# Performance work log

Hardware: AMD Instinct MI355X
Metric: run time of the kernel (lower is better)

## Reference

```python
import jax, jax.numpy as jnp
import numpy as np

N = 50000      # nodes
E = 800000     # edges (avg degree 16)
C = 32         # channels per degree (deg0 and deg1)
HRAD = 32      # radial MLP hidden
L = 4          # attention layers (plus 1 output layer)
HEADS = 4
EPS = 1e-6
NRAD = 7 * C   # rk00, rk10, rv00, rv10, rv11, rv01, rv11b


def setup_inputs() -> dict:
    key = jax.random.key(0)
    ks = jax.random.split(key, 16)
    L1 = L + 1
    s = 0.1
    return {
        "pos": jax.random.normal(ks[0], (N, 3), jnp.float32),
        "f0": jax.random.normal(ks[1], (N, C), jnp.float32),
        "f1": jax.random.normal(ks[2], (N, C, 3), jnp.float32),
        "src": jax.random.randint(ks[3], (E,), 0, N, jnp.int32),
        "dst": jax.random.randint(ks[4], (E,), 0, N, jnp.int32),
        "W1": jax.random.normal(ks[5], (L1, 1, HRAD), jnp.float32) * s,
        "b1": jnp.zeros((L1, HRAD), jnp.float32),
        "W2": jax.random.normal(ks[6], (L1, HRAD, NRAD), jnp.float32) * s,
        "b2": jnp.zeros((L1, NRAD), jnp.float32),
        "Wq": jax.random.normal(ks[7], (L1, C, C), jnp.float32) * s,
        "Wo0": jax.random.normal(ks[8], (L1, C, C), jnp.float32) * s,
        "Wo1": jax.random.normal(ks[9], (L1, C, C), jnp.float32) * s,
        "Ws0": jax.random.normal(ks[10], (L1, C, C), jnp.float32) * s,
        "Ws1": jax.random.normal(ks[11], (L1, C, C), jnp.float32) * s,
        "bg": jnp.zeros((L, C), jnp.float32),
    }


def _attn_layer(f0, f1, u, rlen, src, dst, n, heads,
                W1, b1, W2, b2, Wq, Wo0, Wo1, Ws0, Ws1):
    # radial network, channel-wise modulation per interaction path
    h = jax.nn.relu(rlen[:, None] @ W1 + b1)            # [E, HRAD]
    R = h @ W2 + b2                                     # [E, 7C]
    rk00, rk10, rv00, rv10, rv11, rv01, rv11b = jnp.split(R, 7, axis=-1)
    f0s = f0[src]                                       # [E, C]
    f1s = f1[src]                                       # [E, C, 3]
    dot1 = jnp.einsum('ecd,ed->ec', f1s, u)             # deg1 -> invariant [E, C]
    # equivariant keys (deg0) and values (deg0 + deg1)
    k0 = rk00 * f0s + rk10 * dot1                       # [E, C]
    v0 = rv00 * f0s + rv10 * dot1                       # [E, C]
    v1 = rv11[..., None] * f1s + (rv01 * f0s + rv11b * dot1)[..., None] * u[:, None, :]  # [E, C, 3]
    # multi-head attention logits on invariants
    ch = C // heads
    q = (f0 @ Wq)[dst].reshape(-1, heads, ch)           # [E, H, ch]
    kh = k0.reshape(-1, heads, ch)
    logits = (q * kh).sum(-1) / np.sqrt(ch)             # [E, H]
    # segment softmax over incoming edges of each dst node
    m = jax.ops.segment_max(logits, dst, num_segments=n)
    e = jnp.exp(logits - m[dst])
    z = jax.ops.segment_sum(e, dst, num_segments=n)
    alpha = e / (z[dst] + EPS)                          # [E, H]
    ac = jnp.repeat(alpha, ch, axis=1)                  # [E, C]
    o0 = jax.ops.segment_sum(ac * v0, dst, num_segments=n)                  # [N, C]
    o1 = jax.ops.segment_sum(ac[..., None] * v1, dst, num_segments=n)       # [N, C, 3]
    # self-interaction + skip
    out0 = o0 @ Wo0 + f0 @ Ws0
    out1 = jnp.einsum('ncd,ce->ned', o1, Wo1) + jnp.einsum('ncd,ce->ned', f1, Ws1)
    return out0, out1


def _forward(pos, f0, f1, src, dst, W1, b1, W2, b2, Wq, Wo0, Wo1, Ws0, Ws1, bg):
    n = f0.shape[0]
    # edge-wise basis (l=0,1 spherical harmonics ~ unit direction) and radial distance
    rel = pos[dst] - pos[src]                           # [E, 3]
    rlen = jnp.linalg.norm(rel, axis=-1)                # [E]
    u = rel / (rlen + EPS)[:, None]                     # [E, 3]
    for i in range(L):
        f0, f1 = _attn_layer(f0, f1, u, rlen, src, dst, n, HEADS,
                             W1[i], b1[i], W2[i], b2[i], Wq[i],
                             Wo0[i], Wo1[i], Ws0[i], Ws1[i])
        # GProjRelu: relu on invariants, norm-gated relu on deg-1
        f0 = jax.nn.relu(f0)
        n1 = jnp.linalg.norm(f1, axis=-1)               # [N, C]
        f1 = f1 * (jax.nn.relu(n1 + bg[i]) / (n1 + EPS))[..., None]
    # final output layer: single head, no nonlinearity
    f0, f1 = _attn_layer(f0, f1, u, rlen, src, dst, n, 1,
                         W1[L], b1[L], W2[L], b2[L], Wq[L],
                         Wo0[L], Wo1[L], Ws0[L], Ws1[L])
    return f0, f1


def reference(pos, f0, f1, src, dst, W1, b1, W2, b2, Wq, Wo0, Wo1, Ws0, Ws1, bg):
    return _forward(pos, f0, f1, src, dst, W1, b1, W2, b2, Wq, Wo0, Wo1, Ws0, Ws1, bg)
```

## Files before the change

kernel.cpp:

```cpp
#include <hip/hip_runtime.h>
#include <math.h>

#define CCH 32
#define NCH 224
#define NIV 33
#define HRAD 32
#define ET 16
#define DG1 48


__global__ void hist_kernel(const int* __restrict__ dst, int* __restrict__ counts, int E) {
  int e = blockIdx.x * 256 + threadIdx.x;
  if (e < E) atomicAdd(&counts[dst[e]], 1);
}

__global__ void scan1_kernel(const int* __restrict__ counts, int* __restrict__ offs,
                             int* __restrict__ bsums, int n) {
  __shared__ int sd[1024];
  int t = threadIdx.x;
  int i = blockIdx.x * 1024 + t;
  int v = (i < n) ? counts[i] : 0;
  sd[t] = v;
  __syncthreads();
  for (int o = 1; o < 1024; o <<= 1) {
    int add = (t >= o) ? sd[t - o] : 0;
    __syncthreads();
    sd[t] += add;
    __syncthreads();
  }
  if (i < n) offs[i] = sd[t] - v;
  if (t == 1023) bsums[blockIdx.x] = sd[1023];
}

__global__ void scan2_kernel(int* bsums, int nb) {
  if (threadIdx.x == 0 && blockIdx.x == 0) {
    int acc = 0;
    for (int i = 0; i < nb; i++) { int v = bsums[i]; bsums[i] = acc; acc += v; }
  }
}

__global__ void scan3_kernel(int* __restrict__ offs, const int* __restrict__ bsums,
                             int* __restrict__ cursor, int n, int E) {
  int i = blockIdx.x * 256 + threadIdx.x;
  if (i < n) {
    int v = offs[i] + bsums[i >> 10];
    offs[i] = v;
    cursor[i] = v;
  } else if (i == n) {
    offs[n] = E;
  }
}

__global__ void scatter_kernel(const float* __restrict__ pos, const int* __restrict__ src,
                               const int* __restrict__ dst, int* __restrict__ cursor,
                               int* __restrict__ esrcS, float4* __restrict__ egeoS, int E) {
  int e = blockIdx.x * 256 + threadIdx.x;
  if (e >= E) return;
  int s = src[e], d = dst[e];
  float rx = pos[d * 3 + 0] - pos[s * 3 + 0];
  float ry = pos[d * 3 + 1] - pos[s * 3 + 1];
  float rz = pos[d * 3 + 2] - pos[s * 3 + 2];
  float rl = sqrtf(rx * rx + ry * ry + rz * rz);
  float inv = 1.0f / (rl + 1e-6f);
  int p = atomicAdd(&cursor[d], 1);
  esrcS[p] = s;
  egeoS[p] = make_float4(rx * inv, ry * inv, rz * inv, rl);
}


__global__ void deghistA_kernel(const int* __restrict__ counts, int* __restrict__ bbase,
                                int n, int cpb) {
  __shared__ int lh[256];
  int t = threadIdx.x;
  lh[t] = 0;
  __syncthreads();
  int s = blockIdx.x * cpb, e = s + cpb; if (e > n) e = n;
  for (int i = s + t; i < e; i += 256) {
    int d = counts[i]; d = d > 255 ? 255 : d;
    atomicAdd(&lh[d], 1);
  }
  __syncthreads();
  bbase[blockIdx.x * 256 + t] = lh[t];
}

__global__ void degscanB_kernel(int* __restrict__ bbase) {
  __shared__ int sM[DG1 * 256];
  __shared__ int gb[256];
  int t = threadIdx.x;
  for (int i = t; i < DG1 * 256; i += 256) sM[i] = bbase[i];
  __syncthreads();
  int tot = 0;
  for (int b = 0; b < DG1; b++) tot += sM[b * 256 + t];
  gb[t] = tot;
  __syncthreads();
  if (t == 0) {
    int acc = 0;
    for (int d = 255; d >= 0; --d) { int v = gb[d]; gb[d] = acc; acc += v; }
  }
  __syncthreads();
  int run = gb[t];
  for (int b = 0; b < DG1; b++) { int v = sM[b * 256 + t]; sM[b * 256 + t] = run; run += v; }
  __syncthreads();
  for (int i = t; i < DG1 * 256; i += 256) bbase[i] = sM[i];
}

__global__ void degscatC_kernel(const int* __restrict__ counts, const int* __restrict__ bbase,
                                int* __restrict__ perm, int n, int cpb) {
  __shared__ int lc[256];
  int t = threadIdx.x;
  lc[t] = bbase[blockIdx.x * 256 + t];
  __syncthreads();
  int s = blockIdx.x * cpb, e = s + cpb; if (e > n) e = n;
  for (int i = s + t; i < e; i += 256) {
    int d = counts[i]; d = d > 255 ? 255 : d;
    int p = atomicAdd(&lc[d], 1);
    perm[p] = i;
  }
}


__global__ void pwl_build_kernel(const float* __restrict__ W1, const float* __restrict__ b1,
                                 const float* __restrict__ W2, const float* __restrict__ b2,
                                 float2* __restrict__ coef, float* __restrict__ tks) {
  int l = blockIdx.x / NIV;
  int iv = blockIdx.x - l * NIV;
  int tid = threadIdx.x;
  const float* w1 = W1 + l * HRAD;
  const float* bb1 = b1 + l * HRAD;
  const float* w2 = W2 + l * HRAD * NCH;
  const float* bb2 = b2 + l * NCH;
  __shared__ float a_s[HRAD], b_s[HRAD], t_s[HRAD], t_sorted[HRAD];
  if (tid < HRAD) {
    float a = w1[tid], b = bb1[tid];
    a_s[tid] = a; b_s[tid] = b;
    t_s[tid] = (a != 0.0f) ? (-b / a) : 1e30f;
  }
  __syncthreads();
  if (tid < HRAD) {
    float tj = t_s[tid];
    int rank = 0;
    for (int k = 0; k < HRAD; k++) {
      float tk = t_s[k];
      rank += (tk < tj) || (tk == tj && k < tid);
    }
    t_sorted[rank] = tj;
    if (iv == 0) tks[l * HRAD + tid] = tj;
  }
  __syncthreads();
  if (tid < NCH) {
    int k = tid;
    double lo = (iv == 0) ? (double)t_sorted[0] - 1.0 : (double)t_sorted[iv - 1];
    double hi = (iv == NIV - 1) ? (double)t_sorted[HRAD - 1] + 1.0 : (double)t_sorted[iv];
    double rm = 0.5 * (lo + hi);
    if (iv == 0) rm = (double)t_sorted[0] - 1.0;
    if (iv == NIV - 1) rm = (double)t_sorted[HRAD - 1] + 1.0;
    float alpha = bb2[k];
    float beta = 0.0f;
    for (int j = 0; j < HRAD; j++) {
      if ((double)a_s[j] * rm + (double)b_s[j] > 0.0) {
        float w = w2[j * NCH + k];
        alpha = fmaf(w, b_s[j], alpha);
        beta = fmaf(w, a_s[j], beta);
      }
    }
    coef[l * (NIV * NCH) + iv * NCH + (k & 31) * 7 + (k >> 5)] = make_float2(alpha, beta);
  }
}


__global__ __launch_bounds__(512) void pack_kernel(
    const float* __restrict__ f0, const float* __restrict__ f1,
    const float* __restrict__ Wq0, float scale0,
    float4* __restrict__ fpk, float* __restrict__ qbuf, int n) {
  __shared__ float sWq[1024];
  __shared__ float sF0[ET * 32];
  int tid = threadIdx.x;
  for (int i = tid; i < 1024; i += 512) sWq[i] = Wq0[i];
  __syncthreads();
  int nl = tid >> 5, c = tid & 31;
  for (int base = blockIdx.x * ET; base < n; base += gridDim.x * ET) {
    int node = base + nl;
    float v0 = 0.f, x = 0.f, y = 0.f, z = 0.f;
    if (node < n) {
      v0 = f0[(size_t)node * 32 + c];
      size_t b = ((size_t)node * 32 + c) * 3;
      x = f1[b]; y = f1[b + 1]; z = f1[b + 2];
      fpk[(size_t)node * 32 + c] = make_float4(v0, x, y, z);
    }
    sF0[nl * 32 + c] = v0;
    __syncthreads();
    if (node < n) {
      float q = 0.f;
#pragma unroll
      for (int k = 0; k < 32; k++) q = fmaf(sF0[nl * 32 + k], sWq[k * 32 + c], q);
      qbuf[(size_t)node * 32 + c] = q * scale0;
    }
    __syncthreads();
  }
}


template<int CTRL>
__device__ __forceinline__ float dpp_xor_add(float t) {
  return t + __int_as_float(__builtin_amdgcn_update_dpp(
      0, __float_as_int(t), CTRL, 0xF, 0xF, true));
}

template<int CH>
__global__ __launch_bounds__(1024) void node_kernel(
    const float4* __restrict__ fpk, const float* __restrict__ qbuf,
    float4* __restrict__ Opk,
    const int* __restrict__ esrcS, const float4* __restrict__ egeoS,
    const int* __restrict__ offs, const int* __restrict__ perm,
    const float2* __restrict__ coefG, const float* __restrict__ tkG,
    int n) {
  __shared__ float2 sCoef[NIV * NCH];
  __shared__ float sTk[CCH];
  int tid = threadIdx.x;
  for (int i = tid; i < NIV * NCH; i += 1024) sCoef[i] = coefG[i];
  if (tid < CCH) sTk[tid] = tkG[tid];
  __syncthreads();

  int lane = tid & 63;
  int wid = tid >> 6;
  int c = lane & 31;
  int half = lane >> 5;
  float tk_c = sTk[c];

  int W = gridDim.x * 16;
  int gw = blockIdx.x * 16 + wid;

  int pos0 = gw;
  int pos1 = 2 * W - 1 - gw;
  int pos2 = 2 * W + gw;
  int kk = 2;

  int pcur = (pos0 < n) ? perm[pos0] : 0;
  int pnext = (pos1 < n) ? perm[pos1] : 0;
  int start = 0, end = 0;
  float qs = 0.f;
  int pA = 0;
  float4 pgA = make_float4(0, 0, 0, 0);
  if (pos0 < n) {
    start = offs[pcur];
    end = offs[pcur + 1];
    qs = qbuf[pcur * 32 + c];
    int j0 = start + half;
    if (j0 < end) { pA = esrcS[j0]; pgA = egeoS[j0]; }
  }

  for (; pos0 < n; ) {
    int pnn = (pos2 < n) ? perm[pos2] : 0;
    int nstart = 0, nend = 0;
    float nqs = 0.f;
    if (pos1 < n) {
      nstart = offs[pnext];
      nend = offs[pnext + 1];
      nqs = qbuf[pnext * 32 + c];
    }

    float z = 0.0f;
    float o0 = 0.0f, o10 = 0.0f, o11 = 0.0f, o12 = 0.0f;

    int j = start + half;
    int sB = 0;
    float4 gA = pgA, gB = make_float4(0, 0, 0, 0);
    float4 FA = make_float4(0, 0, 0, 0);
    if (j < end) {
      FA = fpk[pA * 32 + c];
    }
    if (j + 2 < end) { sB = esrcS[j + 2]; gB = egeoS[j + 2]; }

    unsigned long long msk = __ballot(gA.w > tk_c);
    int iv = half ? (int)__popcll(msk >> 32) : (int)__popcll(msk & 0xFFFFFFFFull);
    const float2* cf = sCoef + (iv * 32 + c) * 7;
    float2 cq0 = cf[0], cq1 = cf[1], cq2 = cf[2], cq3 = cf[3];
    float2 cq4 = cf[4], cq5 = cf[5], cq6 = cf[6];

    while (j < end) {
      float4 g = gA;
      float4 F = FA;
      float2 q0 = cq0, q1 = cq1, q2 = cq2, q3 = cq3;
      float2 q4 = cq4, q5 = cq5, q6 = cq6;
      int j2 = j + 2;
      if (j2 < end) {
        FA = fpk[sB * 32 + c];
        gA = gB;
        if (j2 + 2 < end) { sB = esrcS[j2 + 2]; gB = egeoS[j2 + 2]; }
      }
      msk = __ballot(gA.w > tk_c);
      iv = half ? (int)__popcll(msk >> 32) : (int)__popcll(msk & 0xFFFFFFFFull);
      cf = sCoef + (iv * 32 + c) * 7;
      cq0 = cf[0]; cq1 = cf[1]; cq2 = cf[2]; cq3 = cf[3];
      cq4 = cf[4]; cq5 = cf[5]; cq6 = cf[6];

      float r = g.w;
      float rk00 = fmaf(q0.y, r, q0.x), rk10 = fmaf(q1.y, r, q1.x);
      float rv00 = fmaf(q2.y, r, q2.x), rv10 = fmaf(q3.y, r, q3.x);
      float rv11 = fmaf(q4.y, r, q4.x), rv01 = fmaf(q5.y, r, q5.x);
      float rv11b = fmaf(q6.y, r, q6.x);
      float dot1 = fmaf(F.y, g.x, fmaf(F.z, g.y, F.w * g.z));
      float k0 = fmaf(rk00, F.x, rk10 * dot1);
      float t = qs * k0;
      t = dpp_xor_add<0xB1>(t);
      t = dpp_xor_add<0x4E>(t);
      t = dpp_xor_add<0x141>(t);
      if constexpr (CH == 32) {
        t = dpp_xor_add<0x140>(t);
        t = t + __int_as_float(__builtin_amdgcn_ds_swizzle(
                __float_as_int(t), 0x401F));
      }
      float p = __builtin_amdgcn_exp2f(t);
      z += p;
      float v0 = fmaf(rv00, F.x, rv10 * dot1);
      float sg = fmaf(rv01, F.x, rv11b * dot1);
      o0  = fmaf(p, v0, o0);
      o10 = fmaf(p, fmaf(rv11, F.y, sg * g.x), o10);
      o11 = fmaf(p, fmaf(rv11, F.z, sg * g.y), o11);
      o12 = fmaf(p, fmaf(rv11, F.w, sg * g.z), o12);
      j = j2;
    }

    pA = 0;
    pgA = make_float4(0, 0, 0, 0);
    if (pos1 < n) {
      int nj = nstart + half;
      if (nj < nend) { pA = esrcS[nj]; pgA = egeoS[nj]; }
    }

    float zo  = __shfl_xor(z, 32, 64);
    float p0  = __shfl_xor(o0, 32, 64);
    float p10 = __shfl_xor(o10, 32, 64);
    float p11 = __shfl_xor(o11, 32, 64);
    float p12 = __shfl_xor(o12, 32, 64);
    float zf = z + zo;
    float inv = 1.0f / (zf + 1e-6f);
    if (!half) {
      Opk[pcur * 32 + c] = make_float4(
          (o0 + p0) * inv,
          (o10 + p10) * inv,
          (o11 + p11) * inv,
          (o12 + p12) * inv);
    }

    pcur = pnext;
    pnext = pnn;
    start = nstart;
    end = nend;
    qs = nqs;
    pos0 = pos1;
    pos1 = pos2;
    ++kk;
    pos2 = kk * W + ((kk & 1) ? (W - 1 - gw) : gw);
  }
}


__global__ __launch_bounds__(512) void epi_kernel(
    const float4* __restrict__ Opk, float4* __restrict__ fpk,
    const float* __restrict__ Wo0G, const float* __restrict__ Ws0G,
    const float* __restrict__ Wo1G, const float* __restrict__ Ws1G,
    const float* __restrict__ bgG,
    const float* __restrict__ WqN, float* __restrict__ qbuf, float scaleN,
    float* __restrict__ out0, float* __restrict__ out1,
    int mode, int n) {
  __shared__ float4 sW[32 * 32];
  __shared__ float  sWq[32 * 32];
  __shared__ float4 sO[ET * 32];
  __shared__ float4 sF[ET * 32];
  __shared__ float  sF0[ET * 32];
  int tid = threadIdx.x;
  for (int i = tid; i < 1024; i += 512) {
    sW[i] = make_float4(Wo0G[i], Ws0G[i], Wo1G[i], Ws1G[i]);
    if (mode == 0) sWq[i] = WqN[i];
  }
  __syncthreads();
  int nl = tid >> 5;
  int c  = tid & 31;
  for (int base = blockIdx.x * ET; base < n; base += gridDim.x * ET) {
    int node = base + nl;
    bool valid = node < n;
    if (valid) {
      sO[tid] = Opk[(size_t)node * 32 + c];
      sF[tid] = fpk[(size_t)node * 32 + c];
    }
    __syncthreads();
    float a0 = 0.f, ax = 0.f, ay = 0.f, az = 0.f;
#pragma unroll
    for (int k = 0; k < 32; k++) {
      float4 O = sO[nl * 32 + k];
      float4 F = sF[nl * 32 + k];
      float4 w = sW[k * 32 + c];
      a0 = fmaf(O.x, w.x, fmaf(F.x, w.y, a0));
      ax = fmaf(O.y, w.z, fmaf(F.y, w.w, ax));
      ay = fmaf(O.z, w.z, fmaf(F.z, w.w, ay));
      az = fmaf(O.w, w.z, fmaf(F.w, w.w, az));
    }
    if (mode == 0) {
      float f0n = fmaxf(a0, 0.f);
      float n1 = sqrtf(fmaf(ax, ax, fmaf(ay, ay, az * az)));
      float gate = fmaxf(n1 + bgG[c], 0.f) / (n1 + 1e-6f);
      if (valid) fpk[(size_t)node * 32 + c] = make_float4(f0n, ax * gate, ay * gate, az * gate);
      sF0[nl * 32 + c] = f0n;
      __syncthreads();
      if (valid) {
        float q = 0.f;
#pragma unroll
        for (int k = 0; k < 32; k++) q = fmaf(sF0[nl * 32 + k], sWq[k * 32 + c], q);
        qbuf[(size_t)node * 32 + c] = q * scaleN;
      }
      __syncthreads();
    } else {
      if (valid) {
        out0[(size_t)node * 32 + c] = a0;
        size_t b = ((size_t)node * 32 + c) * 3;
        out1[b] = ax; out1[b + 1] = ay; out1[b + 2] = az;
      }
      __syncthreads();
    }
  }
}


extern "C" void kernel_launch(void* const* d_in, const int* in_sizes, int n_in,
                              void* d_out, int out_size, void* d_ws, size_t ws_size,
                              hipStream_t stream) {
  const float* pos = (const float*)d_in[0];
  const float* f0  = (const float*)d_in[1];
  const float* f1  = (const float*)d_in[2];
  const int* src   = (const int*)d_in[3];
  const int* dst   = (const int*)d_in[4];
  const float* W1  = (const float*)d_in[5];
  const float* b1  = (const float*)d_in[6];
  const float* W2  = (const float*)d_in[7];
  const float* b2  = (const float*)d_in[8];
  const float* Wq  = (const float*)d_in[9];
  const float* Wo0 = (const float*)d_in[10];
  const float* Wo1 = (const float*)d_in[11];
  const float* Ws0 = (const float*)d_in[12];
  const float* Ws1 = (const float*)d_in[13];
  const float* bg  = (const float*)d_in[14];

  int N = in_sizes[0] / 3;
  int E = in_sizes[3];

  char* p = (char*)d_ws;
  auto alloc = [&](size_t bytes) {
    char* r = p;
    p += (bytes + 255) & ~(size_t)255;
    return r;
  };
  int* counts   = (int*)alloc((size_t)N * 4);
  int* offs     = (int*)alloc((size_t)(N + 1) * 4);
  int* cursor   = (int*)alloc((size_t)N * 4);
  int* bsums    = (int*)alloc(1024 * 4);
  int* esrcS    = (int*)alloc((size_t)E * 4);
  float4* egeoS = (float4*)alloc((size_t)E * 16);
  float2* coef  = (float2*)alloc((size_t)5 * NIV * NCH * 8);
  float* tks    = (float*)alloc((size_t)5 * HRAD * 4);
  float4* fpk   = (float4*)alloc((size_t)N * CCH * 16);
  float4* Opk   = (float4*)alloc((size_t)N * CCH * 16);
  float* qbuf   = (float*)alloc((size_t)N * CCH * 4);
  int* bbase    = (int*)alloc((size_t)DG1 * 256 * 4);
  int* perm     = (int*)alloc((size_t)N * 4);

  int cpb = (N + DG1 - 1) / DG1;

  pwl_build_kernel<<<5 * NIV, 256, 0, stream>>>(W1, b1, W2, b2, coef, tks);
  hipMemsetAsync(counts, 0, (size_t)N * 4, stream);
  hist_kernel<<<(E + 255) / 256, 256, 0, stream>>>(dst, counts, E);
  deghistA_kernel<<<DG1, 256, 0, stream>>>(counts, bbase, N, cpb);
  int nb = (N + 1023) / 1024;
  scan1_kernel<<<nb, 1024, 0, stream>>>(counts, offs, bsums, N);
  scan2_kernel<<<1, 64, 0, stream>>>(bsums, nb);
  scan3_kernel<<<(N + 1 + 255) / 256, 256, 0, stream>>>(offs, bsums, cursor, N, E);
  degscanB_kernel<<<1, 256, 0, stream>>>(bbase);
  degscatC_kernel<<<DG1, 256, 0, stream>>>(counts, bbase, perm, N, cpb);
  scatter_kernel<<<(E + 255) / 256, 256, 0, stream>>>(pos, src, dst, cursor, esrcS, egeoS, E);

  const float LOG2E = 1.4426950408889634f;
  float sc8 = LOG2E / sqrtf(8.0f);
  float sc32 = LOG2E / sqrtf(32.0f);
  int nblk = (N + ET - 1) / ET;
  pack_kernel<<<nblk, 512, 0, stream>>>(f0, f1, Wq, sc8, fpk, qbuf, N);

  float* out0 = (float*)d_out;
  float* out1 = out0 + (size_t)N * CCH;
  for (int l = 0; l < 5; l++) {
    bool last = (l == 4);
    if (last) {
      node_kernel<32><<<512, 1024, 0, stream>>>(
          fpk, qbuf, Opk, esrcS, egeoS, offs, perm,
          coef + (size_t)l * NIV * NCH, tks + l * HRAD, N);
    } else {
      node_kernel<8><<<512, 1024, 0, stream>>>(
          fpk, qbuf, Opk, esrcS, egeoS, offs, perm,
          coef + (size_t)l * NIV * NCH, tks + l * HRAD, N);
    }
    epi_kernel<<<nblk, 512, 0, stream>>>(
        Opk, fpk,
        Wo0 + l * CCH * CCH, Ws0 + l * CCH * CCH,
        Wo1 + l * CCH * CCH, Ws1 + l * CCH * CCH,
        bg + (last ? 0 : l) * CCH,
        Wq + (l + 1 <= 4 ? (l + 1) : 4) * CCH * CCH, qbuf,
        (l + 1 == 4) ? sc32 : sc8,
        out0, out1, last ? 1 : 0, N);
  }
}
```

Before: 776.0 us.

## Precompute per-edge radial interval indices for all layers in scatter

The scatter kernel now counts, for every edge and each of the five layers, how many radial-MLP breakpoints its length exceeds. It packs these five 6-bit interval indices next to the source index in an int2 array. The node kernel then reads the interval index directly instead of doing a per-edge ballot and popcount against per-channel thresholds. It also evaluates the piecewise-linear radial coefficients one edge ahead in the software pipeline, which trims the critical path of the inner loop. The cost is a larger per-edge record (8 bytes instead of 4) and extra comparison work in the one-time scatter pass.

```diff
diff --git a/kernel.cpp b/kernel.cpp
--- a/kernel.cpp
+++ b/kernel.cpp
@@ -51,10 +51,16 @@
   }
 }
 
+
 __global__ void scatter_kernel(const float* __restrict__ pos, const int* __restrict__ src,
                                const int* __restrict__ dst, int* __restrict__ cursor,
-                               int* __restrict__ esrcS, float4* __restrict__ egeoS, int E) {
-  int e = blockIdx.x * 256 + threadIdx.x;
+                               const float* __restrict__ tksAll,
+                               int2* __restrict__ epkS, float4* __restrict__ egeoS, int E) {
+  __shared__ float sT[5 * HRAD];
+  int t = threadIdx.x;
+  if (t < 5 * HRAD) sT[t] = tksAll[t];
+  __syncthreads();
+  int e = blockIdx.x * 256 + t;
   if (e >= E) return;
   int s = src[e], d = dst[e];
   float rx = pos[d * 3 + 0] - pos[s * 3 + 0];
@@ -62,8 +68,16 @@
   float rz = pos[d * 3 + 2] - pos[s * 3 + 2];
   float rl = sqrtf(rx * rx + ry * ry + rz * rz);
   float inv = 1.0f / (rl + 1e-6f);
+  int ivpk = 0;
+#pragma unroll
+  for (int l = 0; l < 5; l++) {
+    int cnt = 0;
+#pragma unroll
+    for (int k = 0; k < HRAD; k++) cnt += (rl > sT[l * HRAD + k]) ? 1 : 0;
+    ivpk |= cnt << (6 * l);
+  }
   int p = atomicAdd(&cursor[d], 1);
-  esrcS[p] = s;
+  epkS[p] = make_int2(s, ivpk);
   egeoS[p] = make_float4(rx * inv, ry * inv, rz * inv, rl);
 }
 
@@ -210,22 +224,19 @@
 __global__ __launch_bounds__(1024) void node_kernel(
     const float4* __restrict__ fpk, const float* __restrict__ qbuf,
     float4* __restrict__ Opk,
-    const int* __restrict__ esrcS, const float4* __restrict__ egeoS,
+    const int2* __restrict__ epkS, const float4* __restrict__ egeoS,
     const int* __restrict__ offs, const int* __restrict__ perm,
-    const float2* __restrict__ coefG, const float* __restrict__ tkG,
+    const float2* __restrict__ coefG, int ivshift,
     int n) {
   __shared__ float2 sCoef[NIV * NCH];
-  __shared__ float sTk[CCH];
   int tid = threadIdx.x;
   for (int i = tid; i < NIV * NCH; i += 1024) sCoef[i] = coefG[i];
-  if (tid < CCH) sTk[tid] = tkG[tid];
   __syncthreads();
 
   int lane = tid & 63;
   int wid = tid >> 6;
   int c = lane & 31;
   int half = lane >> 5;
-  float tk_c = sTk[c];
 
   int W = gridDim.x * 16;
   int gw = blockIdx.x * 16 + wid;
@@ -239,14 +250,14 @@
   int pnext = (pos1 < n) ? perm[pos1] : 0;
   int start = 0, end = 0;
   float qs = 0.f;
-  int pA = 0;
-  float4 pgA = make_float4(0, 0, 0, 0);
+  int2 pe = make_int2(0, 0);
+  float4 pg = make_float4(0, 0, 0, 0);
   if (pos0 < n) {
     start = offs[pcur];
     end = offs[pcur + 1];
     qs = qbuf[pcur * 32 + c];
     int j0 = start + half;
-    if (j0 < end) { pA = esrcS[j0]; pgA = egeoS[j0]; }
+    if (j0 < end) { pe = epkS[j0]; pg = egeoS[j0]; }
   }
 
   for (; pos0 < n; ) {
@@ -263,45 +274,50 @@
     float o0 = 0.0f, o10 = 0.0f, o11 = 0.0f, o12 = 0.0f;
 
     int j = start + half;
-    int sB = 0;
-    float4 gA = pgA, gB = make_float4(0, 0, 0, 0);
-    float4 FA = make_float4(0, 0, 0, 0);
+
+    float4 g = pg;
+    float4 F = make_float4(0, 0, 0, 0);
+    float R0 = 0, R1 = 0, R2 = 0, R3 = 0, R4 = 0, R5 = 0, R6 = 0;
+    int2 e1 = make_int2(0, 0);
+    float4 g1 = make_float4(0, 0, 0, 0);
     if (j < end) {
-      FA = fpk[pA * 32 + c];
-    }
-    if (j + 2 < end) { sB = esrcS[j + 2]; gB = egeoS[j + 2]; }
-
-    unsigned long long msk = __ballot(gA.w > tk_c);
-    int iv = half ? (int)__popcll(msk >> 32) : (int)__popcll(msk & 0xFFFFFFFFull);
-    const float2* cf = sCoef + (iv * 32 + c) * 7;
-    float2 cq0 = cf[0], cq1 = cf[1], cq2 = cf[2], cq3 = cf[3];
-    float2 cq4 = cf[4], cq5 = cf[5], cq6 = cf[6];
+      F = fpk[pe.x * 32 + c];
+      int iv = (pe.y >> ivshift) & 63;
+      const float2* cf = sCoef + (iv * 32 + c) * 7;
+      float r = g.w;
+      R0 = fmaf(cf[0].y, r, cf[0].x);
+      R1 = fmaf(cf[1].y, r, cf[1].x);
+      R2 = fmaf(cf[2].y, r, cf[2].x);
+      R3 = fmaf(cf[3].y, r, cf[3].x);
+      R4 = fmaf(cf[4].y, r, cf[4].x);
+      R5 = fmaf(cf[5].y, r, cf[5].x);
+      R6 = fmaf(cf[6].y, r, cf[6].x);
+    }
+    if (j + 2 < end) { e1 = epkS[j + 2]; g1 = egeoS[j + 2]; }
 
     while (j < end) {
-      float4 g = gA;
-      float4 F = FA;
-      float2 q0 = cq0, q1 = cq1, q2 = cq2, q3 = cq3;
-      float2 q4 = cq4, q5 = cq5, q6 = cq6;
+      float4 gc = g;
+      float4 Fc = F;
+      float r0 = R0, r1 = R1, r2 = R2, r3 = R3, r4 = R4, r5 = R5, r6 = R6;
       int j2 = j + 2;
       if (j2 < end) {
-        FA = fpk[sB * 32 + c];
-        gA = gB;
-        if (j2 + 2 < end) { sB = esrcS[j2 + 2]; gB = egeoS[j2 + 2]; }
+        F = fpk[e1.x * 32 + c];
+        int iv = (e1.y >> ivshift) & 63;
+        const float2* cf = sCoef + (iv * 32 + c) * 7;
+        float r = g1.w;
+        R0 = fmaf(cf[0].y, r, cf[0].x);
+        R1 = fmaf(cf[1].y, r, cf[1].x);
+        R2 = fmaf(cf[2].y, r, cf[2].x);
+        R3 = fmaf(cf[3].y, r, cf[3].x);
+        R4 = fmaf(cf[4].y, r, cf[4].x);
+        R5 = fmaf(cf[5].y, r, cf[5].x);
+        R6 = fmaf(cf[6].y, r, cf[6].x);
+        g = g1;
+        if (j2 + 2 < end) { e1 = epkS[j2 + 2]; g1 = egeoS[j2 + 2]; }
       }
-      msk = __ballot(gA.w > tk_c);
-      iv = half ? (int)__popcll(msk >> 32) : (int)__popcll(msk & 0xFFFFFFFFull);
-      cf = sCoef + (iv * 32 + c) * 7;
-      cq0 = cf[0]; cq1 = cf[1]; cq2 = cf[2]; cq3 = cf[3];
-      cq4 = cf[4]; cq5 = cf[5]; cq6 = cf[6];
-
-      float r = g.w;
-      float rk00 = fmaf(q0.y, r, q0.x), rk10 = fmaf(q1.y, r, q1.x);
-      float rv00 = fmaf(q2.y, r, q2.x), rv10 = fmaf(q3.y, r, q3.x);
-      float rv11 = fmaf(q4.y, r, q4.x), rv01 = fmaf(q5.y, r, q5.x);
-      float rv11b = fmaf(q6.y, r, q6.x);
-      float dot1 = fmaf(F.y, g.x, fmaf(F.z, g.y, F.w * g.z));
-      float k0 = fmaf(rk00, F.x, rk10 * dot1);
-      float t = qs * k0;
+
+      float dot1 = fmaf(Fc.y, gc.x, fmaf(Fc.z, gc.y, Fc.w * gc.z));
+      float t = qs * fmaf(r0, Fc.x, r1 * dot1);
       t = dpp_xor_add<0xB1>(t);
       t = dpp_xor_add<0x4E>(t);
       t = dpp_xor_add<0x141>(t);
@@ -312,20 +328,20 @@
       }
       float p = __builtin_amdgcn_exp2f(t);
       z += p;
-      float v0 = fmaf(rv00, F.x, rv10 * dot1);
-      float sg = fmaf(rv01, F.x, rv11b * dot1);
+      float v0 = fmaf(r2, Fc.x, r3 * dot1);
+      float sg = fmaf(r5, Fc.x, r6 * dot1);
       o0  = fmaf(p, v0, o0);
-      o10 = fmaf(p, fmaf(rv11, F.y, sg * g.x), o10);
-      o11 = fmaf(p, fmaf(rv11, F.z, sg * g.y), o11);
-      o12 = fmaf(p, fmaf(rv11, F.w, sg * g.z), o12);
+      o10 = fmaf(p, fmaf(r4, Fc.y, sg * gc.x), o10);
+      o11 = fmaf(p, fmaf(r4, Fc.z, sg * gc.y), o11);
+      o12 = fmaf(p, fmaf(r4, Fc.w, sg * gc.z), o12);
       j = j2;
     }
 
-    pA = 0;
-    pgA = make_float4(0, 0, 0, 0);
+    pe = make_int2(0, 0);
+    pg = make_float4(0, 0, 0, 0);
     if (pos1 < n) {
       int nj = nstart + half;
-      if (nj < nend) { pA = esrcS[nj]; pgA = egeoS[nj]; }
+      if (nj < nend) { pe = epkS[nj]; pg = egeoS[nj]; }
     }
 
     float zo  = __shfl_xor(z, 32, 64);
@@ -454,7 +470,7 @@
   int* offs     = (int*)alloc((size_t)(N + 1) * 4);
   int* cursor   = (int*)alloc((size_t)N * 4);
   int* bsums    = (int*)alloc(1024 * 4);
-  int* esrcS    = (int*)alloc((size_t)E * 4);
+  int2* epkS    = (int2*)alloc((size_t)E * 8);
   float4* egeoS = (float4*)alloc((size_t)E * 16);
   float2* coef  = (float2*)alloc((size_t)5 * NIV * NCH * 8);
   float* tks    = (float*)alloc((size_t)5 * HRAD * 4);
@@ -476,7 +492,8 @@
   scan3_kernel<<<(N + 1 + 255) / 256, 256, 0, stream>>>(offs, bsums, cursor, N, E);
   degscanB_kernel<<<1, 256, 0, stream>>>(bbase);
   degscatC_kernel<<<DG1, 256, 0, stream>>>(counts, bbase, perm, N, cpb);
-  scatter_kernel<<<(E + 255) / 256, 256, 0, stream>>>(pos, src, dst, cursor, esrcS, egeoS, E);
+  scatter_kernel<<<(E + 255) / 256, 256, 0, stream>>>(pos, src, dst, cursor, tks,
+                                                      epkS, egeoS, E);
 
   const float LOG2E = 1.4426950408889634f;
   float sc8 = LOG2E / sqrtf(8.0f);
@@ -490,12 +507,12 @@
     bool last = (l == 4);
     if (last) {
       node_kernel<32><<<512, 1024, 0, stream>>>(
-          fpk, qbuf, Opk, esrcS, egeoS, offs, perm,
-          coef + (size_t)l * NIV * NCH, tks + l * HRAD, N);
+          fpk, qbuf, Opk, epkS, egeoS, offs, perm,
+          coef + (size_t)l * NIV * NCH, 6 * l, N);
     } else {
       node_kernel<8><<<512, 1024, 0, stream>>>(
-          fpk, qbuf, Opk, esrcS, egeoS, offs, perm,
-          coef + (size_t)l * NIV * NCH, tks + l * HRAD, N);
+          fpk, qbuf, Opk, epkS, egeoS, offs, perm,
+          coef + (size_t)l * NIV * NCH, 6 * l, N);
     }
     epi_kernel<<<nblk, 512, 0, stream>>>(
         Opk, fpk,
```

Result: faster. 754.9 us (median of 2 runs) (-2.7%).
